# Optimization experiments

Hardware: AMD Instinct MI355X
Metric: run time of the kernel (lower is better)

## Reference

```python
import jax, jax.numpy as jnp
import numpy as np

B, S, H = 4, 2048, 1024
DECAY_RATE = 0.5  # MemoryModule decay: exp(-decay_rate * k), k=1 (most recent pattern)


def setup_inputs() -> dict:
    key = jax.random.key(0)
    ks = jax.random.split(key, 7)
    hidden_states = jax.random.normal(ks[0], (B, S, H), dtype=jnp.float32)
    # past attention pattern: valid row-stochastic attention probs [B, S, S]
    pa = jax.random.uniform(ks[1], (B, S, S), dtype=jnp.float32)
    past_attention = pa / pa.sum(-1, keepdims=True)
    scale = 1.0 / np.sqrt(H).astype(np.float32)
    Wq = jax.random.normal(ks[2], (H, H), dtype=jnp.float32) * scale
    Wk = jax.random.normal(ks[3], (H, H), dtype=jnp.float32) * scale
    Wv = jax.random.normal(ks[4], (H, H), dtype=jnp.float32) * scale
    Wm = jax.random.normal(ks[5], (H, H), dtype=jnp.float32) * scale
    w_gate = jax.random.normal(ks[6], (H,), dtype=jnp.float32) * scale
    return {"hidden_states": hidden_states, "past_attention": past_attention,
            "Wq": Wq, "Wk": Wk, "Wv": Wv, "Wm": Wm, "w_gate": w_gate}


def reference(hidden_states, past_attention, Wq, Wk, Wv, Wm, w_gate):
    h = hidden_states.shape[-1]
    inv_sqrt_h = 1.0 / (h ** 0.5)
    # QKV projections (hidden -> hidden)
    q = jnp.einsum('bsh,hd->bsd', hidden_states, Wq)
    k = jnp.einsum('bsh,hd->bsd', hidden_states, Wk)
    v = jnp.einsum('bsh,hd->bsd', hidden_states, Wv)
    # base attention scores QK^T / sqrt(H)
    scores = jnp.einsum('bqd,bkd->bqk', q, k) * inv_sqrt_h
    # --- memory bias ---
    # decayed history pattern (single most-recent entry, k=1)
    memory = past_attention * jnp.exp(jnp.float32(-DECAY_RATE * 1.0))  # [B,S,S]
    # per-token scalar gate from query
    gates = jax.nn.sigmoid(jnp.einsum('bsh,h->bs', q, w_gate))  # [B,S]
    memory_values = jnp.einsum('bqk,bkd->bqd', memory, v)        # memory @ V
    transformed = jnp.einsum('bsh,hd->bsd', memory_values, Wm)   # memory_transform (no bias)
    gated_memory = gates[..., None] * transformed
    memory_bias = jnp.einsum('bqd,bkd->bqk', gated_memory, k) * inv_sqrt_h
    # augmented attention
    probs = jax.nn.softmax(scores + memory_bias, axis=-1)
    context = jnp.einsum('bqk,bkd->bqd', probs, v)
    return context
```

## Files before the change

kernel.cpp:

```cpp
#include <hip/hip_runtime.h>
#include <hip/hip_bf16.h>

typedef __attribute__((ext_vector_type(4))) float f32x4;
typedef __attribute__((ext_vector_type(8))) __bf16 bf16x8;

__device__ __forceinline__ unsigned short f2bf(float f) {
    union { float f; unsigned u; } x; x.f = f;
    unsigned r = x.u + 0x7fffu + ((x.u >> 16) & 1u);
    return (unsigned short)(r >> 16);
}
__device__ __forceinline__ float bf2f(unsigned short b) {
    union { unsigned u; float f; } x; x.u = ((unsigned)b) << 16;
    return x.f;
}

__device__ __forceinline__ void gload16(const void* g, void* l) {
    __builtin_amdgcn_global_load_lds(
        (const __attribute__((address_space(1))) unsigned int*)g,
        (__attribute__((address_space(3))) unsigned int*)l,
        16, 0, 0);
}

template <int N> __device__ __forceinline__ void vm_wait();
template <> __device__ __forceinline__ void vm_wait<0>() { asm volatile("s_waitcnt vmcnt(0)" ::: "memory"); }
template <> __device__ __forceinline__ void vm_wait<2>() { asm volatile("s_waitcnt vmcnt(2)" ::: "memory"); }
template <> __device__ __forceinline__ void vm_wait<4>() { asm volatile("s_waitcnt vmcnt(4)" ::: "memory"); }

__global__ __launch_bounds__(256) void k_wg2(const float* __restrict__ Wq,
                                             const float* __restrict__ wg,
                                             float* __restrict__ wg2) {
    int lane = threadIdx.x & 63;
    int row = blockIdx.x * 4 + (threadIdx.x >> 6);
    const float4* a = reinterpret_cast<const float4*>(Wq + (size_t)row * 1024);
    const float4* x = reinterpret_cast<const float4*>(wg);
    float s = 0.f;
    for (int i = lane; i < 256; i += 64) {
        float4 av = a[i], bv = x[i];
        s += av.x * bv.x + av.y * bv.y + av.z * bv.z + av.w * bv.w;
    }
#pragma unroll
    for (int o = 1; o < 64; o <<= 1) s += __shfl_xor(s, o);
    if (lane == 0) wg2[row] = s;
}

__global__ __launch_bounds__(256) void k_prep(
    const float* __restrict__ hs, const float* __restrict__ pa,
    const float* __restrict__ Wq, const float* __restrict__ Wk,
    const float* __restrict__ Wv, const float* __restrict__ Wm,
    unsigned short* __restrict__ hs_bf, unsigned short* __restrict__ pa_bf,
    unsigned short* __restrict__ WT, float decay,
    const float* __restrict__ wg2, float* __restrict__ gates) {
    __shared__ float tile[32][33];
    __shared__ float red[8];
    unsigned b = blockIdx.x;
    int t = threadIdx.x;
    if (b < 4096u) {
        float4 v[4];
#pragma unroll
        for (int j = 0; j < 4; ++j)
            v[j] = reinterpret_cast<const float4*>(pa)[b * 1024 + j * 256 + t];
#pragma unroll
        for (int j = 0; j < 4; ++j) {
            union { unsigned short u[4]; uint2 q; } o;
            o.u[0] = f2bf(v[j].x * decay); o.u[1] = f2bf(v[j].y * decay);
            o.u[2] = f2bf(v[j].z * decay); o.u[3] = f2bf(v[j].w * decay);
            reinterpret_cast<uint2*>(pa_bf)[b * 1024 + j * 256 + t] = o.q;
        }
    } else if (b < 8192u) {
        unsigned rp = (b - 4096u) * 2;
        float4 v0 = reinterpret_cast<const float4*>(hs)[rp * 256 + t];
        float4 v1 = reinterpret_cast<const float4*>(hs)[(rp + 1) * 256 + t];
        union { unsigned short u[4]; uint2 q; } o0, o1;
        o0.u[0] = f2bf(v0.x); o0.u[1] = f2bf(v0.y); o0.u[2] = f2bf(v0.z); o0.u[3] = f2bf(v0.w);
        o1.u[0] = f2bf(v1.x); o1.u[1] = f2bf(v1.y); o1.u[2] = f2bf(v1.z); o1.u[3] = f2bf(v1.w);
        reinterpret_cast<uint2*>(hs_bf)[rp * 256 + t] = o0.q;
        reinterpret_cast<uint2*>(hs_bf)[(rp + 1) * 256 + t] = o1.q;
        float4 w = reinterpret_cast<const float4*>(wg2)[t];
        float s0 = v0.x * w.x + v0.y * w.y + v0.z * w.z + v0.w * w.w;
        float s1 = v1.x * w.x + v1.y * w.y + v1.z * w.z + v1.w * w.w;
#pragma unroll
        for (int o2 = 1; o2 < 64; o2 <<= 1) {
            s0 += __shfl_xor(s0, o2);
            s1 += __shfl_xor(s1, o2);
        }
        if ((t & 63) == 0) { red[t >> 6] = s0; red[4 + (t >> 6)] = s1; }
        __syncthreads();
        if (t == 0) {
            float ss = red[0] + red[1] + red[2] + red[3];
            gates[rp] = 1.f / (1.f + __expf(-ss));
        } else if (t == 64) {
            float ss = red[4] + red[5] + red[6] + red[7];
            gates[rp + 1] = 1.f / (1.f + __expf(-ss));
        }
    } else {
        unsigned bb = b - 8192u;
        int z = bb >> 10, rem = bb & 1023;
        int bx = rem & 31, by = rem >> 5;
        const float* src = z == 0 ? Wq : z == 1 ? Wk : z == 2 ? Wv : Wm;
        unsigned short* dst = WT + (size_t)z * 1024 * 1024;
        int lx = t & 31, ly8 = t >> 5;
        int x = bx * 32 + lx;
#pragma unroll
        for (int i = 0; i < 4; i++)
            tile[ly8 + i * 8][lx] = src[(size_t)(by * 32 + ly8 + i * 8) * 1024 + x];
        __syncthreads();
        int tx = by * 32 + lx;
#pragma unroll
        for (int i = 0; i < 4; i++)
            dst[(size_t)(bx * 32 + ly8 + i * 8) * 1024 + tx] = f2bf(tile[lx][ly8 + i * 8]);
    }
}

template <int BN>
struct Geo {
    static constexpr int WN = BN / 64;
    static constexpr int WM = 8 / WN;
    static constexpr int WROWS = 256 / WM;
    static constexpr int MF = WROWS / 16;
    static constexpr int MP = MF / 4;
    static constexpr int ASZ = 256 * 64 * 2;
    static constexpr int BSZ = BN * 64 * 2;
    static constexpr int BUFSZ = ASZ + BSZ;
};

#define GPH(BUFOFF, MB, LB, STG, VMW)                                                   \
    {                                                                                   \
        const char* aB = smem + (BUFOFF);                                               \
        const char* bB = aB + G::ASZ;                                                   \
        bf16x8 af[G::MP * 2];                                                           \
        _Pragma("unroll") for (int mm = 0; mm < G::MP; ++mm)                            \
        _Pragma("unroll") for (int kk = 0; kk < 2; ++kk) {                              \
            int rowx = wrow + ((MB) + mm) * 16 + fr;                                    \
            int slot = (kk * 4 + kq) ^ (rowx & 7);                                      \
            af[mm * 2 + kk] = *reinterpret_cast<const bf16x8*>(aB + rowx * 128 + slot * 16); \
        }                                                                               \
        if (LB) {                                                                       \
            _Pragma("unroll") for (int nn = 0; nn < 4; ++nn)                            \
            _Pragma("unroll") for (int kk = 0; kk < 2; ++kk) {                          \
                int rowx = wcol + nn * 16 + fr;                                         \
                int slot = (kk * 4 + kq) ^ (rowx & 7);                                  \
                bfrag[nn * 2 + kk] = *reinterpret_cast<const bf16x8*>(bB + rowx * 128 + slot * 16); \
            }                                                                           \
        }                                                                               \
        STG;                                                                            \
        __builtin_amdgcn_sched_barrier(0);                                              \
        VMW;                                                                            \
        __builtin_amdgcn_s_barrier();                                                   \
        asm volatile("s_waitcnt lgkmcnt(0)" ::: "memory");                              \
        __builtin_amdgcn_sched_barrier(0);                                              \
        __builtin_amdgcn_s_setprio(1);                                                  \
        _Pragma("unroll") for (int mm = 0; mm < G::MP; ++mm)                            \
        _Pragma("unroll") for (int nn = 0; nn < 4; ++nn)                                \
        _Pragma("unroll") for (int kk = 0; kk < 2; ++kk)                                \
            acc[(MB) + mm][nn] = __builtin_amdgcn_mfma_f32_16x16x32_bf16(               \
                af[mm * 2 + kk], bfrag[nn * 2 + kk], acc[(MB) + mm][nn], 0, 0, 0);      \
        __builtin_amdgcn_s_setprio(0);                                                  \
        __builtin_amdgcn_sched_barrier(0);                                              \
        __builtin_amdgcn_s_barrier();                                                   \
        __builtin_amdgcn_sched_barrier(0);                                              \
    }

template <int EPI, int BN>
__device__ __forceinline__ void gemm_body(
    char* smem,
    const unsigned short* __restrict__ A, int ldA, long long bsA,
    const unsigned short* __restrict__ Bt, int ldB, long long bsB,
    void* __restrict__ Cv, int ldC, long long bsC,
    const unsigned short* __restrict__ Qm, int ldQ,
    const float* __restrict__ gates, float alpha, int K,
    int NX, int NY, int NB, int yf) {
    using G = Geo<BN>;
    const int NT = K >> 6, NI = K >> 7;

    unsigned b = blockIdx.x;
    unsigned wg = (b & 7) * (gridDim.x >> 3) + (b >> 3);
    int xT, yT, zB;
    if (yf) {
        yT = wg % NY; unsigned r2 = wg / NY;
        xT = r2 % NX; zB = (int)(r2 / NX) % NB;
    } else {
        xT = wg % NX; unsigned r2 = wg / NX;
        yT = r2 % NY; zB = (int)(r2 / NY) % NB;
    }

    const unsigned short* Ab = A + (size_t)zB * (size_t)bsA;
    const unsigned short* Bb = Bt + (size_t)zB * (size_t)bsB;

    int t = threadIdx.x, lane = t & 63, wave = t >> 6;
    int wc = wave % G::WN, wr = wave / G::WN;
    int fr = lane & 15, kq = lane >> 4;
    int wrow = wr * G::WROWS, wcol = wc * 64;
    int trow = t >> 3, csx = (t & 7) ^ (trow & 7);
    long long rowTile = (long long)yT * 256, colTile = (long long)xT * BN;

    f32x4 acc[G::MF][4];
#pragma unroll
    for (int m = 0; m < G::MF; ++m)
#pragma unroll
        for (int n = 0; n < 4; ++n) acc[m][n] = (f32x4){0.f, 0.f, 0.f, 0.f};
    bf16x8 bfrag[8];

    auto stageA = [&](int buf, int h, int tt) {
        int kt = tt < NT ? tt : NT - 1;
#pragma unroll
        for (int rr = 0; rr < 2; ++rr) {
            const unsigned short* src =
                Ab + (size_t)(rowTile + h * 128 + rr * 64 + trow) * (size_t)ldA + kt * 64 + csx * 8;
            gload16(src, smem + buf * G::BUFSZ + h * 16384 + rr * 8192 + t * 16);
        }
    };
    auto stageB = [&](int buf, int h, int tt) {
        int kt = tt < NT ? tt : NT - 1;
        if (BN == 256) {
#pragma unroll
            for (int rr = 0; rr < 2; ++rr) {
                const unsigned short* src =
                    Bb + (size_t)(colTile + h * 128 + rr * 64 + trow) * (size_t)ldB + kt * 64 + csx * 8;
                gload16(src, smem + buf * G::BUFSZ + G::ASZ + h * 16384 + rr * 8192 + t * 16);
            }
        } else {
            const unsigned short* src =
                Bb + (size_t)(colTile + h * 64 + trow) * (size_t)ldB + kt * 64 + csx * 8;
            gload16(src, smem + buf * G::BUFSZ + G::ASZ + h * 8192 + t * 16);
        }
    };

    stageA(0, 0, 0); stageA(0, 1, 0);
    stageB(0, 0, 0); stageB(0, 1, 0);
    stageB(1, 0, 1); stageB(1, 1, 1);
    __builtin_amdgcn_sched_barrier(0);
    vm_wait<0>();
    __builtin_amdgcn_s_barrier();
    __builtin_amdgcn_sched_barrier(0);

    constexpr int VMN = (BN == 256) ? 4 : 2;
    for (int i = 0; i < NI; ++i) {
        int t1 = 2 * i + 1, t2 = 2 * i + 2, t3 = 2 * i + 3;
        GPH(0,          0,         1, stageA(1, 0, t1), (void)0);
        GPH(0,          G::MP,     0, stageA(1, 1, t1), (void)0);
        GPH(0,          2 * G::MP, 0, stageB(0, 0, t2), (void)0);
        GPH(0,          3 * G::MP, 0, stageB(0, 1, t2), vm_wait<VMN>());
        GPH(G::BUFSZ,   0,         1, stageA(0, 0, t2), (void)0);
        GPH(G::BUFSZ,   G::MP,     0, stageA(0, 1, t2), (void)0);
        GPH(G::BUFSZ,   2 * G::MP, 0, stageB(1, 0, t3), (void)0);
        GPH(G::BUFSZ,   3 * G::MP, 0, stageB(1, 1, t3), vm_wait<VMN>());
    }
    vm_wait<0>();

    long long rb0 = rowTile + wrow + kq * 4;
    long long cb0 = colTile + wcol + fr;
    if (EPI == 0) {
        unsigned short* C = (unsigned short*)Cv + (size_t)zB * (size_t)bsC;
#pragma unroll
        for (int m = 0; m < G::MF; ++m)
#pragma unroll
            for (int n = 0; n < 4; ++n)
#pragma unroll
                for (int r = 0; r < 4; ++r)
                    C[(size_t)(rb0 + m * 16 + r) * (size_t)ldC + cb0 + n * 16] =
                        f2bf(acc[m][n][r] * alpha);
    } else if (EPI == 1) {
        unsigned short* C = (unsigned short*)Cv;
#pragma unroll
        for (int m = 0; m < G::MF; ++m)
#pragma unroll
            for (int r = 0; r < 4; ++r) {
                long long row = rb0 + m * 16 + r;
                float g = gates[row];
#pragma unroll
                for (int n = 0; n < 4; ++n) {
                    long long col = cb0 + n * 16;
                    float v = (bf2f(Qm[(size_t)row * (size_t)ldQ + col]) + g * acc[m][n][r]) * alpha;
                    C[(size_t)row * (size_t)ldC + col] = f2bf(v);
                }
            }
    } else if (EPI == 4) {
        float* C = (float*)Cv + (size_t)zB * (size_t)bsC;
#pragma unroll
        for (int m = 0; m < G::MF; ++m)
#pragma unroll
            for (int r = 0; r < 4; ++r) {
                long long row = rb0 + m * 16 + r;
                const float4* pp = reinterpret_cast<const float4*>(
                    gates + ((size_t)zB * 2048 + row) * 8);
                float4 p0 = pp[0], p1 = pp[1];
                float g = 1.f / (p0.x + p0.y + p0.z + p0.w + p1.x + p1.y + p1.z + p1.w);
#pragma unroll
                for (int n = 0; n < 4; ++n)
                    C[(size_t)row * (size_t)ldC + cb0 + n * 16] = acc[m][n][r] * g;
            }
    } else if (EPI == 5) {
        unsigned short* C = (unsigned short*)Cv + (size_t)zB * (size_t)bsC;
        float* partials = (float*)gates;
        float srow[G::MF][4];
#pragma unroll
        for (int m = 0; m < G::MF; ++m)
#pragma unroll
            for (int r = 0; r < 4; ++r) srow[m][r] = 0.f;
#pragma unroll
        for (int m = 0; m < G::MF; ++m)
#pragma unroll
            for (int n = 0; n < 4; ++n)
#pragma unroll
                for (int r = 0; r < 4; ++r) {
                    float e = __expf(acc[m][n][r] * alpha);
                    C[(size_t)(rb0 + m * 16 + r) * (size_t)ldC + cb0 + n * 16] = f2bf(e);
                    srow[m][r] += e;
                }
#pragma unroll
        for (int m = 0; m < G::MF; ++m)
#pragma unroll
            for (int r = 0; r < 4; ++r) {
#pragma unroll
                for (int msk = 1; msk < 16; msk <<= 1)
                    srow[m][r] += __shfl_xor(srow[m][r], msk);
            }
        float* sums = (float*)smem;
        if (fr == 0) {
#pragma unroll
            for (int m = 0; m < G::MF; ++m)
#pragma unroll
                for (int r = 0; r < 4; ++r)
                    sums[(wrow + kq * 4 + m * 16 + r) * G::WN + wc] = srow[m][r];
        }
        __syncthreads();
        if (t < 256) {
            float s = 0.f;
#pragma unroll
            for (int j = 0; j < G::WN; ++j) s += sums[t * G::WN + j];
            partials[((size_t)zB * 2048 + (size_t)rowTile + t) * 8 + xT] = s;
        }
    }
}

#define GEMM_ARGS                                                                     \
    const unsigned short *A, int ldA, long long bsA, const unsigned short *Bt,        \
        int ldB, long long bsB, void *Cv, int ldC, long long bsC,                     \
        const unsigned short *Qm, int ldQ, const float *gates, float alpha, int K,    \
        int NX, int NY, int NB, int yf
#define GEMM_PASS A, ldA, bsA, Bt, ldB, bsB, Cv, ldC, bsC, Qm, ldQ, gates, alpha, K, NX, NY, NB, yf

__global__ __launch_bounds__(512, 2) void k_qk(GEMM_ARGS) {
    extern __shared__ char smem[];
    gemm_body<0, 256>(smem, GEMM_PASS);
}
__global__ __launch_bounds__(512, 2) void k_vt(GEMM_ARGS) {
    extern __shared__ char smem[];
    gemm_body<0, 128>(smem, GEMM_PASS);
}
__global__ __launch_bounds__(512, 2) void k_mv(GEMM_ARGS) {
    extern __shared__ char smem[];
    gemm_body<0, 128>(smem, GEMM_PASS);
}
__global__ __launch_bounds__(512, 2) void k_u(GEMM_ARGS) {
    extern __shared__ char smem[];
    gemm_body<1, 128>(smem, GEMM_PASS);
}
__global__ __launch_bounds__(512, 2) void k_logits(GEMM_ARGS) {
    extern __shared__ char smem[];
    gemm_body<5, 256>(smem, GEMM_PASS);
}
__global__ __launch_bounds__(512, 2) void k_ctx(GEMM_ARGS) {
    extern __shared__ char smem[];
    gemm_body<4, 128>(smem, GEMM_PASS);
}

extern "C" void kernel_launch(void* const* d_in, const int* in_sizes, int n_in,
                              void* d_out, int out_size, void* d_ws, size_t ws_size,
                              hipStream_t stream) {
    const float* hs = (const float*)d_in[0];
    const float* pa = (const float*)d_in[1];
    const float* Wq = (const float*)d_in[2];
    const float* Wk = (const float*)d_in[3];
    const float* Wv = (const float*)d_in[4];
    const float* Wm = (const float*)d_in[5];
    const float* wg = (const float*)d_in[6];
    float* out = (float*)d_out;

    const int B = 4, S = 2048, H = 1024;
    const size_t BS = (size_t)B * S;
    const size_t BSH = BS * H;
    const size_t BSS = (size_t)B * S * S;
    const float inv_sqrt_h = 0.03125f;
    const float decay = 0.60653065971263342f;

    char* ws = (char*)d_ws;
    size_t off = 0;
    auto take = [&](size_t bytes) {
        char* p = ws + off;
        off += (bytes + 255) & ~(size_t)255;
        return p;
    };
    unsigned short* hs_bf = (unsigned short*)take(BSH * 2);
    unsigned short* WT    = (unsigned short*)take(4ull * H * H * 2);
    float* wg2            = (float*)take(H * 4);
    float* gates          = (float*)take(BS * 4);
    unsigned short* C2    = (unsigned short*)take(BS * 2 * H * 2);
    unsigned short* v_t   = (unsigned short*)take(BSH * 2);
    unsigned short* pa_bf = (unsigned short*)take(BSS * 2);
    float* partials       = (float*)take(BS * 8 * 4);
    unsigned short* mv    = (unsigned short*)d_out;
    unsigned short* u_bf  = hs_bf;
    unsigned short* probs = pa_bf;
    unsigned short* WvT   = WT + 2ull * H * H;
    unsigned short* WmT   = WT + 3ull * H * H;

    (void)hipFuncSetAttribute((const void*)k_qk,     hipFuncAttributeMaxDynamicSharedMemorySize, 131072);
    (void)hipFuncSetAttribute((const void*)k_vt,     hipFuncAttributeMaxDynamicSharedMemorySize, 98304);
    (void)hipFuncSetAttribute((const void*)k_mv,     hipFuncAttributeMaxDynamicSharedMemorySize, 98304);
    (void)hipFuncSetAttribute((const void*)k_u,      hipFuncAttributeMaxDynamicSharedMemorySize, 98304);
    (void)hipFuncSetAttribute((const void*)k_ctx,    hipFuncAttributeMaxDynamicSharedMemorySize, 98304);
    (void)hipFuncSetAttribute((const void*)k_logits, hipFuncAttributeMaxDynamicSharedMemorySize, 131072);

    k_wg2<<<dim3(256), 256, 0, stream>>>(Wq, wg, wg2);
    k_prep<<<dim3(12288), 256, 0, stream>>>(hs, pa, Wq, Wk, Wv, Wm, hs_bf, pa_bf, WT, decay, wg2, gates);
    k_qk<<<256, 512, 131072, stream>>>(
        hs_bf, H, 0, WT, H, 0, C2, 2 * H, 0, nullptr, 0, nullptr, 1.f, H, 8, 32, 1, 0);
    k_vt<<<256, 512, 98304, stream>>>(
        WvT, H, 0, hs_bf, H, (long long)S * H, v_t, S, (long long)H * S,
        nullptr, 0, nullptr, 1.f, H, 16, 4, 4, 0);
    k_mv<<<256, 512, 98304, stream>>>(
        pa_bf, S, (long long)S * S, v_t, S, (long long)H * S, mv, H, (long long)S * H,
        nullptr, 0, nullptr, 1.f, S, 8, 8, 4, 1);
    k_u<<<256, 512, 98304, stream>>>(
        mv, H, 0, WmT, H, 0, u_bf, H, 0, C2, 2 * H, gates, inv_sqrt_h, H, 8, 32, 1, 0);
    k_logits<<<256, 512, 131072, stream>>>(
        u_bf, H, (long long)S * H, C2 + H, 2 * H, (long long)S * 2 * H,
        probs, S, (long long)S * S, nullptr, 0, partials, 1.f, H, 8, 8, 4, 1);
    k_ctx<<<256, 512, 98304, stream>>>(
        probs, S, (long long)S * S, v_t, S, (long long)H * S, out, H, (long long)S * H,
        nullptr, 0, partials, 1.f, S, 8, 8, 4, 1);
}
```

Measured before the change: 232.0 us.

## Triple-buffer A tiles in GEMM mainloop to deepen prefetch distance

New measurement: 233.1 us. About the same (+0.5%).

```diff
diff --git a/kernel.cpp b/kernel.cpp
--- a/kernel.cpp
+++ b/kernel.cpp
@@ -23,8 +23,8 @@
 
 template <int N> __device__ __forceinline__ void vm_wait();
 template <> __device__ __forceinline__ void vm_wait<0>() { asm volatile("s_waitcnt vmcnt(0)" ::: "memory"); }
-template <> __device__ __forceinline__ void vm_wait<2>() { asm volatile("s_waitcnt vmcnt(2)" ::: "memory"); }
-template <> __device__ __forceinline__ void vm_wait<4>() { asm volatile("s_waitcnt vmcnt(4)" ::: "memory"); }
+template <> __device__ __forceinline__ void vm_wait<6>() { asm volatile("s_waitcnt vmcnt(6)" ::: "memory"); }
+template <> __device__ __forceinline__ void vm_wait<8>() { asm volatile("s_waitcnt vmcnt(8)" ::: "memory"); }
 
 __global__ __launch_bounds__(256) void k_wg2(const float* __restrict__ Wq,
                                              const float* __restrict__ wg,
@@ -120,13 +120,14 @@
     static constexpr int MP = MF / 4;
     static constexpr int ASZ = 256 * 64 * 2;
     static constexpr int BSZ = BN * 64 * 2;
-    static constexpr int BUFSZ = ASZ + BSZ;
+    static constexpr int ABUF3 = 3 * ASZ;
+    static constexpr int VMN = (BN == 256) ? 8 : 6;
 };
 
-#define GPH(BUFOFF, MB, LB, STG, VMW)                                                   \
+#define GPH(AB, BB, MB, LB, STG, VMW)                                                   \
     {                                                                                   \
-        const char* aB = smem + (BUFOFF);                                               \
-        const char* bB = aB + G::ASZ;                                                   \
+        const char* aB = (AB);                                                          \
+        const char* bB = (BB);                                                          \
         bf16x8 af[G::MP * 2];                                                           \
         _Pragma("unroll") for (int mm = 0; mm < G::MP; ++mm)                            \
         _Pragma("unroll") for (int kk = 0; kk < 2; ++kk) {                              \
@@ -200,50 +201,56 @@
         for (int n = 0; n < 4; ++n) acc[m][n] = (f32x4){0.f, 0.f, 0.f, 0.f};
     bf16x8 bfrag[8];
 
-    auto stageA = [&](int buf, int h, int tt) {
+    auto stageA = [&](int tt, int h) {
         int kt = tt < NT ? tt : NT - 1;
+        char* dst = smem + (tt % 3) * G::ASZ + h * 16384;
 #pragma unroll
         for (int rr = 0; rr < 2; ++rr) {
             const unsigned short* src =
                 Ab + (size_t)(rowTile + h * 128 + rr * 64 + trow) * (size_t)ldA + kt * 64 + csx * 8;
-            gload16(src, smem + buf * G::BUFSZ + h * 16384 + rr * 8192 + t * 16);
+            gload16(src, dst + rr * 8192 + t * 16);
         }
     };
-    auto stageB = [&](int buf, int h, int tt) {
+    auto stageB = [&](int tt, int h) {
         int kt = tt < NT ? tt : NT - 1;
+        char* dst = smem + G::ABUF3 + (tt & 1) * G::BSZ;
         if (BN == 256) {
 #pragma unroll
             for (int rr = 0; rr < 2; ++rr) {
                 const unsigned short* src =
                     Bb + (size_t)(colTile + h * 128 + rr * 64 + trow) * (size_t)ldB + kt * 64 + csx * 8;
-                gload16(src, smem + buf * G::BUFSZ + G::ASZ + h * 16384 + rr * 8192 + t * 16);
+                gload16(src, dst + h * 16384 + rr * 8192 + t * 16);
             }
         } else {
             const unsigned short* src =
                 Bb + (size_t)(colTile + h * 64 + trow) * (size_t)ldB + kt * 64 + csx * 8;
-            gload16(src, smem + buf * G::BUFSZ + G::ASZ + h * 8192 + t * 16);
+            gload16(src, dst + h * 8192 + t * 16);
         }
     };
 
-    stageA(0, 0, 0); stageA(0, 1, 0);
-    stageB(0, 0, 0); stageB(0, 1, 0);
-    stageB(1, 0, 1); stageB(1, 1, 1);
+    stageA(0, 0); stageA(0, 1);
+    stageB(0, 0); stageB(0, 1);
+    stageA(1, 0); stageA(1, 1);
+    stageB(1, 0); stageB(1, 1);
     __builtin_amdgcn_sched_barrier(0);
-    vm_wait<0>();
+    vm_wait<G::VMN>();
     __builtin_amdgcn_s_barrier();
     __builtin_amdgcn_sched_barrier(0);
 
-    constexpr int VMN = (BN == 256) ? 4 : 2;
     for (int i = 0; i < NI; ++i) {
-        int t1 = 2 * i + 1, t2 = 2 * i + 2, t3 = 2 * i + 3;
-        GPH(0,          0,         1, stageA(1, 0, t1), (void)0);
-        GPH(0,          G::MP,     0, stageA(1, 1, t1), (void)0);
-        GPH(0,          2 * G::MP, 0, stageB(0, 0, t2), (void)0);
-        GPH(0,          3 * G::MP, 0, stageB(0, 1, t2), vm_wait<VMN>());
-        GPH(G::BUFSZ,   0,         1, stageA(0, 0, t2), (void)0);
-        GPH(G::BUFSZ,   G::MP,     0, stageA(0, 1, t2), (void)0);
-        GPH(G::BUFSZ,   2 * G::MP, 0, stageB(1, 0, t3), (void)0);
-        GPH(G::BUFSZ,   3 * G::MP, 0, stageB(1, 1, t3), vm_wait<VMN>());
+        int t0 = 2 * i, t1 = 2 * i + 1;
+        const char* aB0 = smem + (t0 % 3) * G::ASZ;
+        const char* aB1 = smem + (t1 % 3) * G::ASZ;
+        const char* bB0 = smem + G::ABUF3 + (t0 & 1) * G::BSZ;
+        const char* bB1 = smem + G::ABUF3 + (t1 & 1) * G::BSZ;
+        GPH(aB0, bB0, 0,         1, stageA(t0 + 2, 0), (void)0);
+        GPH(aB0, bB0, G::MP,     0, stageA(t0 + 2, 1), (void)0);
+        GPH(aB0, bB0, 2 * G::MP, 0, stageB(t0 + 2, 0), (void)0);
+        GPH(aB0, bB0, 3 * G::MP, 0, stageB(t0 + 2, 1), vm_wait<G::VMN>());
+        GPH(aB1, bB1, 0,         1, stageA(t1 + 2, 0), (void)0);
+        GPH(aB1, bB1, G::MP,     0, stageA(t1 + 2, 1), (void)0);
+        GPH(aB1, bB1, 2 * G::MP, 0, stageB(t1 + 2, 0), (void)0);
+        GPH(aB1, bB1, 3 * G::MP, 0, stageB(t1 + 2, 1), vm_wait<G::VMN>());
     }
     vm_wait<0>();
 
@@ -405,29 +412,29 @@
     unsigned short* WvT   = WT + 2ull * H * H;
     unsigned short* WmT   = WT + 3ull * H * H;
 
-    (void)hipFuncSetAttribute((const void*)k_qk,     hipFuncAttributeMaxDynamicSharedMemorySize, 131072);
-    (void)hipFuncSetAttribute((const void*)k_vt,     hipFuncAttributeMaxDynamicSharedMemorySize, 98304);
-    (void)hipFuncSetAttribute((const void*)k_mv,     hipFuncAttributeMaxDynamicSharedMemorySize, 98304);
-    (void)hipFuncSetAttribute((const void*)k_u,      hipFuncAttributeMaxDynamicSharedMemorySize, 98304);
-    (void)hipFuncSetAttribute((const void*)k_ctx,    hipFuncAttributeMaxDynamicSharedMemorySize, 98304);
-    (void)hipFuncSetAttribute((const void*)k_logits, hipFuncAttributeMaxDynamicSharedMemorySize, 131072);
+    (void)hipFuncSetAttribute((const void*)k_qk,     hipFuncAttributeMaxDynamicSharedMemorySize, 163840);
+    (void)hipFuncSetAttribute((const void*)k_vt,     hipFuncAttributeMaxDynamicSharedMemorySize, 131072);
+    (void)hipFuncSetAttribute((const void*)k_mv,     hipFuncAttributeMaxDynamicSharedMemorySize, 131072);
+    (void)hipFuncSetAttribute((const void*)k_u,      hipFuncAttributeMaxDynamicSharedMemorySize, 131072);
+    (void)hipFuncSetAttribute((const void*)k_ctx,    hipFuncAttributeMaxDynamicSharedMemorySize, 131072);
+    (void)hipFuncSetAttribute((const void*)k_logits, hipFuncAttributeMaxDynamicSharedMemorySize, 163840);
 
     k_wg2<<<dim3(256), 256, 0, stream>>>(Wq, wg, wg2);
     k_prep<<<dim3(12288), 256, 0, stream>>>(hs, pa, Wq, Wk, Wv, Wm, hs_bf, pa_bf, WT, decay, wg2, gates);
-    k_qk<<<256, 512, 131072, stream>>>(
+    k_qk<<<256, 512, 163840, stream>>>(
         hs_bf, H, 0, WT, H, 0, C2, 2 * H, 0, nullptr, 0, nullptr, 1.f, H, 8, 32, 1, 0);
-    k_vt<<<256, 512, 98304, stream>>>(
+    k_vt<<<256, 512, 131072, stream>>>(
         WvT, H, 0, hs_bf, H, (long long)S * H, v_t, S, (long long)H * S,
         nullptr, 0, nullptr, 1.f, H, 16, 4, 4, 0);
-    k_mv<<<256, 512, 98304, stream>>>(
+    k_mv<<<256, 512, 131072, stream>>>(
         pa_bf, S, (long long)S * S, v_t, S, (long long)H * S, mv, H, (long long)S * H,
         nullptr, 0, nullptr, 1.f, S, 8, 8, 4, 1);
-    k_u<<<256, 512, 98304, stream>>>(
+    k_u<<<256, 512, 131072, stream>>>(
         mv, H, 0, WmT, H, 0, u_bf, H, 0, C2, 2 * H, gates, inv_sqrt_h, H, 8, 32, 1, 0);
-    k_logits<<<256, 512, 131072, stream>>>(
+    k_logits<<<256, 512, 163840, stream>>>(
         u_bf, H, (long long)S * H, C2 + H, 2 * H, (long long)S * 2 * H,
         probs, S, (long long)S * S, nullptr, 0, partials, 1.f, H, 8, 8, 4, 1);
-    k_ctx<<<256, 512, 98304, stream>>>(
+    k_ctx<<<256, 512, 131072, stream>>>(
         probs, S, (long long)S * S, v_t, S, (long long)H * S, out, H, (long long)S * H,
         nullptr, 0, partials, 1.f, S, 8, 8, 4, 1);
 }
```

## Store past attention as scaled FP8 and use dedicated memory-value GEMM kernel

Applied to the files above, without the earlier changes.

After: 252.5 us. 8.8% more time.

```diff
diff --git a/kernel.cpp b/kernel.cpp
--- a/kernel.cpp
+++ b/kernel.cpp
@@ -1,6 +1,7 @@
 #include <hip/hip_runtime.h>
 #include <hip/hip_bf16.h>
 
+typedef __attribute__((ext_vector_type(2))) float f32x2;
 typedef __attribute__((ext_vector_type(4))) float f32x4;
 typedef __attribute__((ext_vector_type(8))) __bf16 bf16x8;
 
@@ -12,6 +13,23 @@
 __device__ __forceinline__ float bf2f(unsigned short b) {
     union { unsigned u; float f; } x; x.u = ((unsigned)b) << 16;
     return x.f;
+}
+
+__device__ __forceinline__ unsigned pk8(float4 v, float sc) {
+    unsigned lo, hi;
+    asm("v_cvt_pk_fp8_f32 %0, %1, %2" : "=v"(lo) : "v"(v.x * sc), "v"(v.y * sc));
+    asm("v_cvt_pk_fp8_f32 %0, %1, %2" : "=v"(hi) : "v"(v.z * sc), "v"(v.w * sc));
+    return (lo & 0xffffu) | (hi << 16);
+}
+__device__ __forceinline__ f32x2 up8(unsigned w) {
+    f32x2 r;
+    asm("v_cvt_pk_f32_fp8 %0, %1" : "=v"(r) : "v"(w));
+    return r;
+}
+__device__ __forceinline__ unsigned pkbf(float lo, float hi) {
+    unsigned r;
+    asm("v_cvt_pk_bf16_f32 %0, %1, %2" : "=v"(r) : "v"(lo), "v"(hi));
+    return r;
 }
 
 __device__ __forceinline__ void gload16(const void* g, void* l) {
@@ -47,25 +65,21 @@
     const float* __restrict__ hs, const float* __restrict__ pa,
     const float* __restrict__ Wq, const float* __restrict__ Wk,
     const float* __restrict__ Wv, const float* __restrict__ Wm,
-    unsigned short* __restrict__ hs_bf, unsigned short* __restrict__ pa_bf,
-    unsigned short* __restrict__ WT, float decay,
+    unsigned short* __restrict__ hs_bf, unsigned char* __restrict__ pa8,
+    unsigned short* __restrict__ WT,
     const float* __restrict__ wg2, float* __restrict__ gates) {
     __shared__ float tile[32][33];
     __shared__ float red[8];
     unsigned b = blockIdx.x;
     int t = threadIdx.x;
     if (b < 4096u) {
-        float4 v[4];
-#pragma unroll
-        for (int j = 0; j < 4; ++j)
-            v[j] = reinterpret_cast<const float4*>(pa)[b * 1024 + j * 256 + t];
-#pragma unroll
-        for (int j = 0; j < 4; ++j) {
-            union { unsigned short u[4]; uint2 q; } o;
-            o.u[0] = f2bf(v[j].x * decay); o.u[1] = f2bf(v[j].y * decay);
-            o.u[2] = f2bf(v[j].z * decay); o.u[3] = f2bf(v[j].w * decay);
-            reinterpret_cast<uint2*>(pa_bf)[b * 1024 + j * 256 + t] = o.q;
-        }
+        size_t base4 = ((size_t)b * 256 + t) * 4;
+        const float4* src = reinterpret_cast<const float4*>(pa);
+        float4 v0 = src[base4], v1 = src[base4 + 1], v2 = src[base4 + 2], v3 = src[base4 + 3];
+        uint4 o;
+        o.x = pk8(v0, 2048.f); o.y = pk8(v1, 2048.f);
+        o.z = pk8(v2, 2048.f); o.w = pk8(v3, 2048.f);
+        reinterpret_cast<uint4*>(pa8)[(size_t)b * 256 + t] = o;
     } else if (b < 8192u) {
         unsigned rp = (b - 4096u) * 2;
         float4 v0 = reinterpret_cast<const float4*>(hs)[rp * 256 + t];
@@ -348,10 +362,6 @@
     extern __shared__ char smem[];
     gemm_body<0, 128>(smem, GEMM_PASS);
 }
-__global__ __launch_bounds__(512, 2) void k_mv(GEMM_ARGS) {
-    extern __shared__ char smem[];
-    gemm_body<0, 128>(smem, GEMM_PASS);
-}
 __global__ __launch_bounds__(512, 2) void k_u(GEMM_ARGS) {
     extern __shared__ char smem[];
     gemm_body<1, 128>(smem, GEMM_PASS);
@@ -363,6 +373,130 @@
 __global__ __launch_bounds__(512, 2) void k_ctx(GEMM_ARGS) {
     extern __shared__ char smem[];
     gemm_body<4, 128>(smem, GEMM_PASS);
+}
+
+#define MV8_PH(BUFOFF, MB, LB, STG, VMW)                                               \
+    {                                                                                  \
+        const char* aB = smem + (BUFOFF);                                              \
+        const char* bB = aB + 16384;                                                   \
+        uint2 w[2];                                                                    \
+        _Pragma("unroll") for (int kk = 0; kk < 2; ++kk) {                             \
+            int rowx = wrow + (MB) * 16 + fr;                                          \
+            int g16 = ((kq >> 1) + kk * 2) ^ ((rowx >> 1) & 3);                        \
+            w[kk] = *reinterpret_cast<const uint2*>(aB + rowx * 64 + g16 * 16 + (kq & 1) * 8); \
+        }                                                                              \
+        if (LB) {                                                                      \
+            _Pragma("unroll") for (int nn = 0; nn < 4; ++nn)                           \
+            _Pragma("unroll") for (int kk = 0; kk < 2; ++kk) {                         \
+                int rowx = wcol + nn * 16 + fr;                                        \
+                int slot = (kk * 4 + kq) ^ (rowx & 7);                                 \
+                bfrag[nn * 2 + kk] = *reinterpret_cast<const bf16x8*>(bB + rowx * 128 + slot * 16); \
+            }                                                                          \
+        }                                                                              \
+        STG;                                                                           \
+        __builtin_amdgcn_sched_barrier(0);                                             \
+        VMW;                                                                           \
+        __builtin_amdgcn_s_barrier();                                                  \
+        asm volatile("s_waitcnt lgkmcnt(0)" ::: "memory");                             \
+        __builtin_amdgcn_sched_barrier(0);                                             \
+        bf16x8 af[2];                                                                  \
+        _Pragma("unroll") for (int kk = 0; kk < 2; ++kk) {                             \
+            f32x2 f0 = up8(w[kk].x), f1 = up8(w[kk].x >> 16);                          \
+            f32x2 f2 = up8(w[kk].y), f3 = up8(w[kk].y >> 16);                          \
+            union { unsigned u[4]; bf16x8 v; } o;                                      \
+            o.u[0] = pkbf(f0.x, f0.y); o.u[1] = pkbf(f1.x, f1.y);                      \
+            o.u[2] = pkbf(f2.x, f2.y); o.u[3] = pkbf(f3.x, f3.y);                      \
+            af[kk] = o.v;                                                              \
+        }                                                                              \
+        __builtin_amdgcn_s_setprio(1);                                                 \
+        _Pragma("unroll") for (int nn = 0; nn < 4; ++nn)                               \
+        _Pragma("unroll") for (int kk = 0; kk < 2; ++kk)                               \
+            acc[(MB)][nn] = __builtin_amdgcn_mfma_f32_16x16x32_bf16(                   \
+                af[kk], bfrag[nn * 2 + kk], acc[(MB)][nn], 0, 0, 0);                   \
+        __builtin_amdgcn_s_setprio(0);                                                 \
+        __builtin_amdgcn_sched_barrier(0);                                             \
+        __builtin_amdgcn_s_barrier();                                                  \
+        __builtin_amdgcn_sched_barrier(0);                                             \
+    }
+
+__global__ __launch_bounds__(512, 2) void k_mv8(
+    const unsigned char* __restrict__ A8,
+    const unsigned short* __restrict__ Bt,
+    unsigned short* __restrict__ C,
+    float alpha) {
+    extern __shared__ char smem[];
+    constexpr int BUFSZ = 32768;
+    const int NT = 32, NI = 16;
+    const int NX = 8, NY = 8, NB = 4;
+
+    unsigned b = blockIdx.x;
+    unsigned wgi = (b & 7) * (gridDim.x >> 3) + (b >> 3);
+    int yT = wgi % NY; unsigned r2 = wgi / NY;
+    int xT = r2 % NX; int zB = (int)(r2 / NX) % NB;
+
+    const unsigned char* Ab = A8 + (size_t)zB * 2048 * 2048;
+    const unsigned short* Bb = Bt + (size_t)zB * 1024 * 2048;
+
+    int t = threadIdx.x, lane = t & 63, wave = t >> 6;
+    int wc = wave & 1, wr = wave >> 1;
+    int fr = lane & 15, kq = lane >> 4;
+    int wrow = wr * 64, wcol = wc * 64;
+    int trow = t >> 3, csx = (t & 7) ^ (trow & 7);
+    int trow8 = t >> 2, csx8 = (t & 3) ^ ((trow8 >> 1) & 3);
+    long long rowTile = (long long)yT * 256, colTile = (long long)xT * 128;
+
+    f32x4 acc[4][4];
+#pragma unroll
+    for (int m = 0; m < 4; ++m)
+#pragma unroll
+        for (int n = 0; n < 4; ++n) acc[m][n] = (f32x4){0.f, 0.f, 0.f, 0.f};
+    bf16x8 bfrag[8];
+
+    auto stageA = [&](int tt, int rr) {
+        int kt = tt < NT ? tt : NT - 1;
+        const unsigned char* src =
+            Ab + (size_t)(rowTile + rr * 128 + trow8) * 2048 + kt * 64 + csx8 * 16;
+        gload16(src, smem + (tt & 1) * BUFSZ + rr * 8192 + t * 16);
+    };
+    auto stageB = [&](int tt, int h) {
+        int kt = tt < NT ? tt : NT - 1;
+        const unsigned short* src =
+            Bb + (size_t)(colTile + h * 64 + trow) * 2048 + kt * 64 + csx * 8;
+        gload16(src, smem + (tt & 1) * BUFSZ + 16384 + h * 8192 + t * 16);
+    };
+
+    stageA(0, 0); stageA(0, 1);
+    stageB(0, 0); stageB(0, 1);
+    stageB(1, 0); stageB(1, 1);
+    __builtin_amdgcn_sched_barrier(0);
+    vm_wait<2>();
+    __builtin_amdgcn_s_barrier();
+    __builtin_amdgcn_sched_barrier(0);
+
+    for (int i = 0; i < NI; ++i) {
+        int t1 = 2 * i + 1, t2 = 2 * i + 2, t3 = 2 * i + 3;
+        MV8_PH(0,      0, 1, stageA(t1, 0), (void)0);
+        MV8_PH(0,      1, 0, stageA(t1, 1), (void)0);
+        MV8_PH(0,      2, 0, stageB(t2, 0), (void)0);
+        MV8_PH(0,      3, 0, stageB(t2, 1), vm_wait<2>());
+        MV8_PH(BUFSZ,  0, 1, stageA(t2, 0), (void)0);
+        MV8_PH(BUFSZ,  1, 0, stageA(t2, 1), (void)0);
+        MV8_PH(BUFSZ,  2, 0, stageB(t3, 0), (void)0);
+        MV8_PH(BUFSZ,  3, 0, stageB(t3, 1), vm_wait<2>());
+    }
+    vm_wait<0>();
+
+    long long rb0 = rowTile + wrow + kq * 4;
+    long long cb0 = colTile + wcol + fr;
+    unsigned short* Cb = C + (size_t)zB * 2048 * 1024;
+#pragma unroll
+    for (int m = 0; m < 4; ++m)
+#pragma unroll
+        for (int n = 0; n < 4; ++n)
+#pragma unroll
+            for (int r = 0; r < 4; ++r)
+                Cb[(size_t)(rb0 + m * 16 + r) * 1024 + cb0 + n * 16] =
+                    f2bf(acc[m][n][r] * alpha);
 }
 
 extern "C" void kernel_launch(void* const* d_in, const int* in_sizes, int n_in,
@@ -397,31 +531,29 @@
     float* gates          = (float*)take(BS * 4);
     unsigned short* C2    = (unsigned short*)take(BS * 2 * H * 2);
     unsigned short* v_t   = (unsigned short*)take(BSH * 2);
-    unsigned short* pa_bf = (unsigned short*)take(BSS * 2);
+    unsigned char* pa8    = (unsigned char*)take(BSS);
+    unsigned short* probs = (unsigned short*)take(BSS * 2);
     float* partials       = (float*)take(BS * 8 * 4);
     unsigned short* mv    = (unsigned short*)d_out;
     unsigned short* u_bf  = hs_bf;
-    unsigned short* probs = pa_bf;
     unsigned short* WvT   = WT + 2ull * H * H;
     unsigned short* WmT   = WT + 3ull * H * H;
 
     (void)hipFuncSetAttribute((const void*)k_qk,     hipFuncAttributeMaxDynamicSharedMemorySize, 131072);
     (void)hipFuncSetAttribute((const void*)k_vt,     hipFuncAttributeMaxDynamicSharedMemorySize, 98304);
-    (void)hipFuncSetAttribute((const void*)k_mv,     hipFuncAttributeMaxDynamicSharedMemorySize, 98304);
+    (void)hipFuncSetAttribute((const void*)k_mv8,    hipFuncAttributeMaxDynamicSharedMemorySize, 65536);
     (void)hipFuncSetAttribute((const void*)k_u,      hipFuncAttributeMaxDynamicSharedMemorySize, 98304);
     (void)hipFuncSetAttribute((const void*)k_ctx,    hipFuncAttributeMaxDynamicSharedMemorySize, 98304);
     (void)hipFuncSetAttribute((const void*)k_logits, hipFuncAttributeMaxDynamicSharedMemorySize, 131072);
 
     k_wg2<<<dim3(256), 256, 0, stream>>>(Wq, wg, wg2);
-    k_prep<<<dim3(12288), 256, 0, stream>>>(hs, pa, Wq, Wk, Wv, Wm, hs_bf, pa_bf, WT, decay, wg2, gates);
+    k_prep<<<dim3(12288), 256, 0, stream>>>(hs, pa, Wq, Wk, Wv, Wm, hs_bf, pa8, WT, wg2, gates);
     k_qk<<<256, 512, 131072, stream>>>(
         hs_bf, H, 0, WT, H, 0, C2, 2 * H, 0, nullptr, 0, nullptr, 1.f, H, 8, 32, 1, 0);
     k_vt<<<256, 512, 98304, stream>>>(
         WvT, H, 0, hs_bf, H, (long long)S * H, v_t, S, (long long)H * S,
         nullptr, 0, nullptr, 1.f, H, 16, 4, 4, 0);
-    k_mv<<<256, 512, 98304, stream>>>(
-        pa_bf, S, (long long)S * S, v_t, S, (long long)H * S, mv, H, (long long)S * H,
-        nullptr, 0, nullptr, 1.f, S, 8, 8, 4, 1);
+    k_mv8<<<256, 512, 65536, stream>>>(pa8, v_t, mv, decay / 2048.f);
     k_u<<<256, 512, 98304, stream>>>(
         mv, H, 0, WmT, H, 0, u_bf, H, 0, C2, 2 * H, gates, inv_sqrt_h, H, 8, 32, 1, 0);
     k_logits<<<256, 512, 131072, stream>>>(
```
